# Kernel optimization log

Measured on AMD Instinct MI355X. Metric: run time of the kernel, lower is better.

The kernel has to match this reference:

```python
import jax, jax.numpy as jnp
import numpy as np

L, B, D = 8192, 4096, 1024


def setup_inputs() -> dict:
    key = jax.random.key(0)
    k1, k2, k3, k4 = jax.random.split(key, 4)
    return {
        "q_hat": jax.random.normal(k1, (L, D), dtype=jnp.float32),
        "q_real": jax.random.normal(k2, (L, D), dtype=jnp.float32),
        "encoded_gt": jax.random.normal(k3, (B, D), dtype=jnp.float32),
        "encoded_pred": jax.random.normal(k4, (B, D), dtype=jnp.float32),
    }


def reference(q_hat, q_real, encoded_gt, encoded_pred):
    # local_loss: -(1/L) * sum_i dot(q_hat[i], q_real[i])
    # (replaces the Python loop of L tiny torch.dot launches with one fused reduce)
    local = -jnp.mean(jnp.sum(q_hat * q_real, axis=-1))

    # global_loss: sum_{i,j} max(0, <pred_i, gt_j> - <pred_i, gt_i> + 1)
    # (replaces the O(B^2) double loop of torch.dot calls with one GEMM)
    scores = jnp.einsum("id,jd->ij", encoded_pred, encoded_gt)  # [B, B]
    pos = jnp.diagonal(scores)                                   # [B]
    margin = jnp.float32(1.0)
    glob = jnp.sum(jnp.maximum(0.0, scores - pos[:, None] + margin))

    return local + glob
```

## Files before the change

### kernel.cpp

```cpp
#include <hip/hip_runtime.h>
#include <hip/hip_bf16.h>

#define LROWS 8192
#define BROWS 4096
#define DDIM  1024

typedef __attribute__((ext_vector_type(4)))  int   i32x4;
typedef __attribute__((ext_vector_type(8)))  int   i32x8;
typedef __attribute__((ext_vector_type(16))) float f32x16;

typedef const unsigned int __attribute__((address_space(1))) gu32;
typedef unsigned int       __attribute__((address_space(3))) su32;

__device__ inline unsigned int pack_fp8x4(float4 v) {
    unsigned int w = 0;
    w = __builtin_amdgcn_cvt_pk_fp8_f32(v.x, v.y, w, false);
    w = __builtin_amdgcn_cvt_pk_fp8_f32(v.z, v.w, w, true);
    return w;
}

__global__ __launch_bounds__(256) void prep_kernel(
    const float4* __restrict__ pred,
    const float4* __restrict__ gt,
    unsigned int* __restrict__ opred,
    unsigned int* __restrict__ ogt,
    const float4* __restrict__ qh,
    const float4* __restrict__ qr,
    float* __restrict__ pos,
    float* __restrict__ lpart,
    float* __restrict__ out) {
    __shared__ float sred[4], sred2[4];
    const int row = blockIdx.x;
    const int t = threadIdx.x;
    if (row == 0 && t == 0) out[0] = 0.0f;

    const int idx = row * 256 + t;
    float4 p = pred[idx];
    float4 g = gt[idx];
    opred[idx] = pack_fp8x4(p);
    ogt[idx]   = pack_fp8x4(g);
    float s = p.x * g.x + p.y * g.y + p.z * g.z + p.w * g.w;

    const int qi = row * 512 + t;
    float4 a0 = qh[qi], b0 = qr[qi];
    float4 a1 = qh[qi + 256], b1 = qr[qi + 256];
    float ls = a0.x * b0.x + a0.y * b0.y + a0.z * b0.z + a0.w * b0.w
             + a1.x * b1.x + a1.y * b1.y + a1.z * b1.z + a1.w * b1.w;

    #pragma unroll
    for (int o = 32; o > 0; o >>= 1) {
        s  += __shfl_down(s, o, 64);
        ls += __shfl_down(ls, o, 64);
    }
    if ((t & 63) == 0) { sred[t >> 6] = s; sred2[t >> 6] = ls; }
    __syncthreads();
    if (t == 0) {
        pos[row]   = sred[0] + sred[1] + sred[2] + sred[3];
        lpart[row] = sred2[0] + sred2[1] + sred2[2] + sred2[3];
    }
}

__global__ __launch_bounds__(512, 2) void hinge_gemm(
    const unsigned char* __restrict__ A,
    const unsigned char* __restrict__ Bm,
    const float* __restrict__ pos,
    const float* __restrict__ lpart,
    float* __restrict__ out) {
    extern __shared__ unsigned char smem[];
    unsigned char* const As = smem;
    unsigned char* const Bs = smem + 65536;
    float* const pos_s = (float*)(smem + 131072);
    float* const sred  = (float*)(smem + 131072 + 1024);

    const int orig = blockIdx.x;
    const int xk = orig & 7, xj = orig >> 3;
    const int bm = (xk >> 1) * 4 + (xj >> 3);
    const int bn = (xk & 1) * 8 + (xj & 7);

    const int tid = threadIdx.x;
    const int lane = tid & 63;
    const int wave = tid >> 6;
    const int wm = wave >> 2;
    const int wn = wave & 3;

    if (tid < 256) pos_s[tid] = pos[bm * 256 + tid];

    const int grow = lane >> 3;
    const int usw  = (lane & 7) ^ grow;

    const unsigned char* Abase = A  + (size_t)(bm * 256) * DDIM;
    const unsigned char* Bbase = Bm + (size_t)(bn * 256) * DDIM;

    f32x16 acc[4][2];
    #pragma unroll
    for (int i = 0; i < 4; i++)
        #pragma unroll
        for (int j = 0; j < 2; j++)
            #pragma unroll
            for (int r = 0; r < 16; r++) acc[i][j][r] = 0.0f;

    const int sc1 = 0x7f7f7f7f;
    const int mrow = lane & 31;
    const int kh = lane >> 5;

    auto stage = [&](int buf, int k0) {
        #pragma unroll
        for (int i = 0; i < 4; i++) {
            const int c = wave * 4 + i;
            const int row = c * 8 + grow;
            __builtin_amdgcn_global_load_lds(
                (gu32*)(Abase + (size_t)row * DDIM + k0 + usw * 16),
                (su32*)(As + buf * 32768 + c * 1024), 16, 0, 0);
            __builtin_amdgcn_global_load_lds(
                (gu32*)(Bbase + (size_t)row * DDIM + k0 + usw * 16),
                (su32*)(Bs + buf * 32768 + c * 1024), 16, 0, 0);
        }
    };

    auto compute = [&](int buf) {
        const unsigned char* Ab = As + buf * 32768;
        const unsigned char* Bb = Bs + buf * 32768;
        #pragma unroll
        for (int h = 0; h < 2; h++) {
            const int u0 = h * 4 + kh * 2;
            i32x8 af[4];
            i32x8 bg[2];
            #pragma unroll
            for (int mt = 0; mt < 4; mt++) {
                const int r = wm * 128 + mt * 32 + mrow;
                i32x4 x0 = *(const i32x4*)&Ab[r * 128 + ((u0    ) ^ (r & 7)) * 16];
                i32x4 x1 = *(const i32x4*)&Ab[r * 128 + ((u0 + 1) ^ (r & 7)) * 16];
                af[mt] = __builtin_shufflevector(x0, x1, 0, 1, 2, 3, 4, 5, 6, 7);
            }
            #pragma unroll
            for (int nt = 0; nt < 2; nt++) {
                const int r = wn * 64 + nt * 32 + mrow;
                i32x4 x0 = *(const i32x4*)&Bb[r * 128 + ((u0    ) ^ (r & 7)) * 16];
                i32x4 x1 = *(const i32x4*)&Bb[r * 128 + ((u0 + 1) ^ (r & 7)) * 16];
                bg[nt] = __builtin_shufflevector(x0, x1, 0, 1, 2, 3, 4, 5, 6, 7);
            }
            __builtin_amdgcn_s_setprio(1);
            #pragma unroll
            for (int mt = 0; mt < 4; mt++)
                #pragma unroll
                for (int nt = 0; nt < 2; nt++)
                    acc[mt][nt] = __builtin_amdgcn_mfma_scale_f32_32x32x64_f8f6f4(
                        af[mt], bg[nt], acc[mt][nt],
                        0, 0,
                        0, sc1,
                        0, sc1);
            __builtin_amdgcn_s_setprio(0);
        }
    };

    stage(0, 0);
    __syncthreads();
    int p = 0;
    for (int t = 0; t < 7; t++) {
        stage(p ^ 1, (t + 1) * 128);
        compute(p);
        __syncthreads();
        p ^= 1;
    }
    compute(p);

    float s = 0.0f;
    const int rq = 4 * kh;
    #pragma unroll
    for (int mt = 0; mt < 4; mt++) {
        #pragma unroll
        for (int nt = 0; nt < 2; nt++) {
            #pragma unroll
            for (int i = 0; i < 16; i++) {
                const int lr = wm * 128 + mt * 32 + (i & 3) + 8 * (i >> 2) + rq;
                const float v = acc[mt][nt][i] - pos_s[lr] + 1.0f;
                s += fmaxf(v, 0.0f);
            }
        }
    }
    #pragma unroll
    for (int o = 32; o > 0; o >>= 1) s += __shfl_down(s, o, 64);
    if (lane == 0) sred[wave] = s;
    __syncthreads();
    if (tid == 0) {
        float tot = 0.0f;
        #pragma unroll
        for (int w = 0; w < 8; w++) tot += sred[w];
        const int bid = (bm * 16 + bn) * 16;
        float lp = 0.0f;
        #pragma unroll
        for (int i = 0; i < 16; i++) lp += lpart[bid + i];
        atomicAdd(out, tot - lp * (1.0f / (float)LROWS));
    }
}

extern "C" void kernel_launch(void* const* d_in, const int* in_sizes, int n_in,
                              void* d_out, int out_size, void* d_ws, size_t ws_size,
                              hipStream_t stream) {
    const float* q_hat  = (const float*)d_in[0];
    const float* q_real = (const float*)d_in[1];
    const float* gt     = (const float*)d_in[2];
    const float* pred   = (const float*)d_in[3];
    float* out = (float*)d_out;

    char* ws = (char*)d_ws;
    unsigned char* pred_8 = (unsigned char*)ws;
    unsigned char* gt_8   = (unsigned char*)(ws + (size_t)BROWS * DDIM);
    float* pos   = (float*)(ws + (size_t)2 * BROWS * DDIM);
    float* lpart = (float*)(ws + (size_t)2 * BROWS * DDIM + BROWS * 4);

    hipLaunchKernelGGL(prep_kernel, dim3(BROWS), dim3(256), 0, stream,
                       (const float4*)pred, (const float4*)gt,
                       (unsigned int*)pred_8, (unsigned int*)gt_8,
                       (const float4*)q_hat, (const float4*)q_real,
                       pos, lpart, out);

    const size_t lds_bytes = 131072 + 1024 + 32;
    hipLaunchKernelGGL(hinge_gemm, dim3(256), dim3(512), lds_bytes, stream,
                       pred_8, gt_8, pos, lpart, out);
}
```

Measured before the change: 138.0 us.

## Move local q_hat·q_real reduction into the GEMM main loop

The local-loss dot product over q_hat and q_real (64 MB of fp32 reads) moves out of the prep kernel and into the hinge GEMM's K-loop. Each GEMM block streams an 8192-float4 slice, prefetched one iteration ahead, and folds it into the per-block reduction. This shrinks the bandwidth-bound prep kernel and aims to hide the q reads behind MFMA compute. In exchange the GEMM needs more registers for the prefetch buffers and shares memory bandwidth with its own LDS staging loads.

New measurement: 131.2 us. 1.05x faster.

```diff
diff --git a/kernel.cpp b/kernel.cpp
--- a/kernel.cpp
+++ b/kernel.cpp
@@ -24,12 +24,9 @@
     const float4* __restrict__ gt,
     unsigned int* __restrict__ opred,
     unsigned int* __restrict__ ogt,
-    const float4* __restrict__ qh,
-    const float4* __restrict__ qr,
     float* __restrict__ pos,
-    float* __restrict__ lpart,
     float* __restrict__ out) {
-    __shared__ float sred[4], sred2[4];
+    __shared__ float sred[4];
     const int row = blockIdx.x;
     const int t = threadIdx.x;
     if (row == 0 && t == 0) out[0] = 0.0f;
@@ -41,36 +38,26 @@
     ogt[idx]   = pack_fp8x4(g);
     float s = p.x * g.x + p.y * g.y + p.z * g.z + p.w * g.w;
 
-    const int qi = row * 512 + t;
-    float4 a0 = qh[qi], b0 = qr[qi];
-    float4 a1 = qh[qi + 256], b1 = qr[qi + 256];
-    float ls = a0.x * b0.x + a0.y * b0.y + a0.z * b0.z + a0.w * b0.w
-             + a1.x * b1.x + a1.y * b1.y + a1.z * b1.z + a1.w * b1.w;
-
-    #pragma unroll
-    for (int o = 32; o > 0; o >>= 1) {
-        s  += __shfl_down(s, o, 64);
-        ls += __shfl_down(ls, o, 64);
-    }
-    if ((t & 63) == 0) { sred[t >> 6] = s; sred2[t >> 6] = ls; }
+    #pragma unroll
+    for (int o = 32; o > 0; o >>= 1) s += __shfl_down(s, o, 64);
+    if ((t & 63) == 0) sred[t >> 6] = s;
     __syncthreads();
-    if (t == 0) {
-        pos[row]   = sred[0] + sred[1] + sred[2] + sred[3];
-        lpart[row] = sred2[0] + sred2[1] + sred2[2] + sred2[3];
-    }
+    if (t == 0) pos[row] = sred[0] + sred[1] + sred[2] + sred[3];
 }
 
 __global__ __launch_bounds__(512, 2) void hinge_gemm(
     const unsigned char* __restrict__ A,
     const unsigned char* __restrict__ Bm,
     const float* __restrict__ pos,
-    const float* __restrict__ lpart,
+    const float4* __restrict__ qh,
+    const float4* __restrict__ qr,
     float* __restrict__ out) {
     extern __shared__ unsigned char smem[];
     unsigned char* const As = smem;
     unsigned char* const Bs = smem + 65536;
     float* const pos_s = (float*)(smem + 131072);
-    float* const sred  = (float*)(smem + 131072 + 1024);
+    float* const sred  = (float*)(smem + 132096);
+    float* const sred2 = (float*)(smem + 132128);
 
     const int orig = blockIdx.x;
     const int xk = orig & 7, xj = orig >> 3;
@@ -90,6 +77,9 @@
 
     const unsigned char* Abase = A  + (size_t)(bm * 256) * DDIM;
     const unsigned char* Bbase = Bm + (size_t)(bn * 256) * DDIM;
+
+    const float4* qhb = qh + (size_t)orig * 8192;
+    const float4* qrb = qr + (size_t)orig * 8192;
 
     f32x16 acc[4][2];
     #pragma unroll
@@ -153,15 +143,29 @@
         }
     };
 
+    float ls = 0.0f;
+    float4 ch0, ch1, cr0, cr1;
+    float4 nh0, nh1, nr0, nr1;
+
     stage(0, 0);
+    ch0 = qhb[tid];       ch1 = qhb[tid + 512];
+    cr0 = qrb[tid];       cr1 = qrb[tid + 512];
     __syncthreads();
     int p = 0;
     for (int t = 0; t < 7; t++) {
         stage(p ^ 1, (t + 1) * 128);
+        const int qo = (t + 1) * 1024 + tid;
+        nh0 = qhb[qo];       nh1 = qhb[qo + 512];
+        nr0 = qrb[qo];       nr1 = qrb[qo + 512];
+        ls += ch0.x * cr0.x + ch0.y * cr0.y + ch0.z * cr0.z + ch0.w * cr0.w
+            + ch1.x * cr1.x + ch1.y * cr1.y + ch1.z * cr1.z + ch1.w * cr1.w;
         compute(p);
         __syncthreads();
+        ch0 = nh0; ch1 = nh1; cr0 = nr0; cr1 = nr1;
         p ^= 1;
     }
+    ls += ch0.x * cr0.x + ch0.y * cr0.y + ch0.z * cr0.z + ch0.w * cr0.w
+        + ch1.x * cr1.x + ch1.y * cr1.y + ch1.z * cr1.z + ch1.w * cr1.w;
     compute(p);
 
     float s = 0.0f;
@@ -179,17 +183,16 @@
         }
     }
     #pragma unroll
-    for (int o = 32; o > 0; o >>= 1) s += __shfl_down(s, o, 64);
-    if (lane == 0) sred[wave] = s;
+    for (int o = 32; o > 0; o >>= 1) {
+        s  += __shfl_down(s, o, 64);
+        ls += __shfl_down(ls, o, 64);
+    }
+    if (lane == 0) { sred[wave] = s; sred2[wave] = ls; }
     __syncthreads();
     if (tid == 0) {
-        float tot = 0.0f;
-        #pragma unroll
-        for (int w = 0; w < 8; w++) tot += sred[w];
-        const int bid = (bm * 16 + bn) * 16;
-        float lp = 0.0f;
-        #pragma unroll
-        for (int i = 0; i < 16; i++) lp += lpart[bid + i];
+        float tot = 0.0f, lp = 0.0f;
+        #pragma unroll
+        for (int w = 0; w < 8; w++) { tot += sred[w]; lp += sred2[w]; }
         atomicAdd(out, tot - lp * (1.0f / (float)LROWS));
     }
 }
@@ -207,15 +210,14 @@
     unsigned char* pred_8 = (unsigned char*)ws;
     unsigned char* gt_8   = (unsigned char*)(ws + (size_t)BROWS * DDIM);
     float* pos   = (float*)(ws + (size_t)2 * BROWS * DDIM);
-    float* lpart = (float*)(ws + (size_t)2 * BROWS * DDIM + BROWS * 4);
 
     hipLaunchKernelGGL(prep_kernel, dim3(BROWS), dim3(256), 0, stream,
                        (const float4*)pred, (const float4*)gt,
                        (unsigned int*)pred_8, (unsigned int*)gt_8,
-                       (const float4*)q_hat, (const float4*)q_real,
-                       pos, lpart, out);
-
-    const size_t lds_bytes = 131072 + 1024 + 32;
+                       pos, out);
+
+    const size_t lds_bytes = 131072 + 1024 + 64;
     hipLaunchKernelGGL(hinge_gemm, dim3(256), dim3(512), lds_bytes, stream,
-                       pred_8, gt_8, pos, lpart, out);
-}
+                       pred_8, gt_8, pos,
+                       (const float4*)q_hat, (const float4*)q_real, out);
+}
```
